# Performance work log

Hardware: AMD Instinct MI355X
Metric: run time of the kernel (lower is better)

## Reference

```python
import jax, jax.numpy as jnp
import numpy as np

K = 1024        # num_embeddings
D = 256         # embedding_dim
B, T = 64, 512  # batch, time -> N = 32768 flattened vectors
S = 5           # num_samples
DECAY = 0.999
EPS = 1e-5
COMMIT = 0.25


def setup_inputs() -> dict:
    key = jax.random.key(0)
    k1, k2 = jax.random.split(key)
    x = jax.random.normal(k1, (B, T, D), dtype=jnp.float32)
    # nn.init.uniform_(weight, -1/512, 1/512)
    embedding = jax.random.uniform(k2, (K, D), dtype=jnp.float32, minval=-1.0 / 512, maxval=1.0 / 512)
    ema_count = jnp.zeros((K,), dtype=jnp.float32)
    ema_weight = embedding  # buffer initialized as a clone of the weight
    return {"x": x, "embedding": embedding, "ema_count": ema_count, "ema_weight": ema_weight}


def reference(x, embedding, ema_count, ema_weight):
    N = x.shape[0] * x.shape[1]
    xf = x.reshape(-1, D)                      # [N, D]
    xf_sg = jax.lax.stop_gradient(xf)
    w = jax.lax.stop_gradient(embedding)       # [K, D]

    distances = (jnp.sum(w * w, axis=1)[None, :]
                 + jnp.sum(xf_sg * xf_sg, axis=1, keepdims=True)
                 - 2.0 * (xf_sg @ w.T))

    # categorical sampling with logits = -distances, S samples per row -> [S, N]
    skey = jax.random.key(42)
    samples = jax.random.categorical(skey, -distances, axis=-1, shape=(S, N))

    # mean of S one-hots without materializing [S, N, K] one-hot tensor
    encodings = jnp.zeros((N, K), dtype=jnp.float32).at[jnp.arange(N)[None, :], samples].add(1.0 / S)

    # EMA codebook update (training path; all under no_grad in torch)
    new_count = DECAY * ema_count + (1.0 - DECAY) * jnp.sum(encodings, axis=0)
    n = jnp.sum(new_count)
    new_count = (new_count + EPS) / (n + K * EPS) * n
    dw = encodings.T @ xf_sg                   # [K, D]
    new_weight = DECAY * ema_weight + (1.0 - DECAY) * dw
    new_embedding = new_weight / new_count[:, None]

    # gather with the UPDATED codebook, mean over samples -> [N, D]
    quantized = jnp.mean(new_embedding[samples], axis=0).reshape(x.shape)
    quantized = jax.lax.stop_gradient(quantized)

    e_latent_loss = jnp.mean((x - quantized) ** 2)
    loss = COMMIT * e_latent_loss

    quantized_st = x + jax.lax.stop_gradient(quantized - x)  # straight-through

    avg_probs = jnp.mean(encodings, axis=0)
    perplexity = jnp.exp(-jnp.sum(avg_probs * jnp.log(avg_probs + 1e-10)))

    return quantized_st, loss, perplexity, new_embedding, new_count, new_weight
```

## Files before the change

kernel.cpp:

```cpp
#include <hip/hip_runtime.h>
#include <stdint.h>
#include <math.h>

#define NV 32768
#define DIM 256
#define KCB 1024
#define NSAMP 5

typedef double f64x4 __attribute__((ext_vector_type(4)));

__device__ __forceinline__ uint32_t rotl32(uint32_t v, int r) {
  return (v << r) | (v >> (32 - r));
}

__device__ __forceinline__ void threefry2x32(uint32_t c0, uint32_t c1,
                                             uint32_t& o0, uint32_t& o1) {
  const uint32_t k0 = 0u, k1 = 42u;
  const uint32_t k2 = k0 ^ k1 ^ 0x1BD11BDAu;
  uint32_t x0 = c0 + k0, x1 = c1 + k1;
  x0 += x1; x1 = rotl32(x1, 13); x1 ^= x0;
  x0 += x1; x1 = rotl32(x1, 15); x1 ^= x0;
  x0 += x1; x1 = rotl32(x1, 26); x1 ^= x0;
  x0 += x1; x1 = rotl32(x1,  6); x1 ^= x0;
  x0 += k1; x1 += k2 + 1u;
  x0 += x1; x1 = rotl32(x1, 17); x1 ^= x0;
  x0 += x1; x1 = rotl32(x1, 29); x1 ^= x0;
  x0 += x1; x1 = rotl32(x1, 16); x1 ^= x0;
  x0 += x1; x1 = rotl32(x1, 24); x1 ^= x0;
  x0 += k2; x1 += k0 + 2u;
  x0 += x1; x1 = rotl32(x1, 13); x1 ^= x0;
  x0 += x1; x1 = rotl32(x1, 15); x1 ^= x0;
  x0 += x1; x1 = rotl32(x1, 26); x1 ^= x0;
  x0 += x1; x1 = rotl32(x1,  6); x1 ^= x0;
  x0 += k0; x1 += k1 + 3u;
  x0 += x1; x1 = rotl32(x1, 17); x1 ^= x0;
  x0 += x1; x1 = rotl32(x1, 29); x1 ^= x0;
  x0 += x1; x1 = rotl32(x1, 16); x1 ^= x0;
  x0 += x1; x1 = rotl32(x1, 24); x1 ^= x0;
  x0 += k1; x1 += k2 + 4u;
  x0 += x1; x1 = rotl32(x1, 13); x1 ^= x0;
  x0 += x1; x1 = rotl32(x1, 15); x1 ^= x0;
  x0 += x1; x1 = rotl32(x1, 26); x1 ^= x0;
  x0 += x1; x1 = rotl32(x1,  6); x1 ^= x0;
  x0 += k2; x1 += k0 + 5u;
  o0 = x0; o1 = x1;
}

__device__ __forceinline__ float neg_log_f32(float xf) {
  uint32_t i = __float_as_uint(xf);
  int e = ((int)(i - 0x3f3504f3u)) >> 23;
  double m = (double)__uint_as_float(i - (uint32_t)(e << 23));
  double z = (m - 1.0) / (m + 1.0);
  double p = z * z;
  double poly = 0x1.1111111111111p-4;
  poly = fma(poly, p, 0x1.3b13b13b13b14p-4);
  poly = fma(poly, p, 0x1.745d1745d1746p-4);
  poly = fma(poly, p, 0x1.c71c71c71c71cp-4);
  poly = fma(poly, p, 0x1.2492492492492p-3);
  poly = fma(poly, p, 0x1.999999999999ap-3);
  poly = fma(poly, p, 0x1.5555555555555p-2);
  poly = fma(poly, p, 1.0);
  double r = fma(-2.0 * z, poly, (double)(-e) * 0x1.62e42fefa39efp-1);
  return (float)r;
}

__device__ __forceinline__ float u_from_bits(uint32_t bits) {
  uint32_t m = bits >> 9;
  return (m == 0u) ? 1.17549435e-38f
                   : (__uint_as_float(m | 0x3f800000u) - 1.0f);
}

__device__ __forceinline__ float gumbel_exact(uint32_t bits) {
  float u = u_from_bits(bits);
  float t = neg_log_f32(u);
  return neg_log_f32(t);
}

__device__ __forceinline__ float gumbel_approx(uint32_t bits) {
  float u = u_from_bits(bits);
  float t = __log2f(u) * (-0.6931471805599453f);
  return __log2f(t) * (-0.6931471805599453f);
}

#define E2G 4e-5f


__global__ __launch_bounds__(256) void k_prep32(const float* __restrict__ emb,
                                                float* __restrict__ wT) {
  __shared__ float tile[64][65];
  int bk = blockIdx.x;
  int bd = blockIdx.y;
  int t = threadIdx.x;
  int tr = t >> 6, tc = t & 63;
#pragma unroll
  for (int i = 0; i < 16; ++i) {
    int kk = tr + i * 4;
    tile[kk][tc] = emb[(size_t)(bk * 64 + kk) * 256 + bd * 64 + tc];
  }
  __syncthreads();
#pragma unroll
  for (int i = 0; i < 16; ++i) {
    int dd = tr + i * 4;
    wT[(size_t)(bd * 64 + dd) * 1024 + bk * 64 + tc] = tile[tc][dd];
  }
}

__global__ __launch_bounds__(256) void k_prep64(const float* __restrict__ emb,
                                                double* __restrict__ wT64) {
  __shared__ float tile[64][65];
  int bk = blockIdx.x;
  int bd = blockIdx.y;
  int t = threadIdx.x;
  int tr = t >> 6, tc = t & 63;
#pragma unroll
  for (int i = 0; i < 16; ++i) {
    int kk = tr + i * 4;
    tile[kk][tc] = emb[(size_t)(bk * 64 + kk) * 256 + bd * 64 + tc];
  }
  __syncthreads();
#pragma unroll
  for (int i = 0; i < 16; ++i) {
    int dd = tr + i * 4;
    wT64[(size_t)(bd * 64 + dd) * 1024 + bk * 64 + tc] = (double)tile[tc][dd];
  }
}

__global__ __launch_bounds__(256) void k_rowsumsq(const float* __restrict__ a,
                                                  float* __restrict__ outp,
                                                  int rows) {
  int r = blockIdx.x * blockDim.x + threadIdx.x;
  if (r >= rows) return;
  const float* p = a + (size_t)r * DIM;
  float acc = 0.0f;
  for (int i = 0; i < DIM; ++i) {
    float pi = p[i];
    acc = __fadd_rn(acc, __fmul_rn(pi, pi));
  }
  outp[r] = acc;
}


__global__ __launch_bounds__(256) void k_logits(const float* __restrict__ x,
                                                const float* __restrict__ wT,
                                                const float* __restrict__ wsum,
                                                const float* __restrict__ xsum,
                                                float* __restrict__ logits,
                                                int chunkbase) {
  __shared__ float xl[32 * 260];
  __shared__ float xs[32];
  int nb = blockIdx.x;
  int t = threadIdx.x;
  int lane = t & 63, wv = t >> 6;
  int m = lane & 15, g = lane >> 4;
  int rg = wv >> 1, chf = wv & 1;

#pragma unroll
  for (int i = 0; i < 32; ++i)
    xl[i * 260 + t] = x[((size_t)(chunkbase + nb * 32) + i) * 256 + t];
  if (t < 32) xs[t] = xsum[chunkbase + nb * 32 + t];
  __syncthreads();

  const float* ap = xl + (rg * 16 + m) * 260 + g;
  for (int ch = 0; ch < 4; ++ch) {
    for (int ct = 0; ct < 8; ++ct) {
      int klocal = chf * 128 + ct * 16 + m;
      int kglob = ch * 256 + klocal;
      f64x4 C = {0.0, 0.0, 0.0, 0.0};
      const float* bp = wT + (size_t)g * 1024 + kglob;
#pragma unroll 8
      for (int step = 0; step < 64; ++step) {
        double a = (double)ap[step * 4];
        double b = (double)bp[(size_t)step * 4096];
        C = __builtin_amdgcn_mfma_f64_16x16x4f64(a, b, C, 0, 0, 0);
      }
      float ws_k = wsum[kglob];
#pragma unroll
      for (int j = 0; j < 4; ++j) {
        int rloc = rg * 16 + g * 4 + j;
        float l32 = __fsub_rn(__fmul_rn(2.0f, (float)C[j]),
                              __fadd_rn(ws_k, xs[rloc]));
        logits[(size_t)(nb * 32 + rloc) * 1024 + kglob] = l32;
      }
    }
  }
}

__global__ __launch_bounds__(256) void k_sampler(const float* __restrict__ logits,
                                                 int* __restrict__ samples,
                                                 int* __restrict__ cnt,
                                                 int chunkbase) {
  int t = threadIdx.x;
  int p = t & 7;
  int rloc = blockIdx.x * 32 + (t >> 3);
  int s = blockIdx.y;
  int row = chunkbase + rloc;
  uint32_t srow = ((uint32_t)s * (uint32_t)NV + (uint32_t)row) * 1024u;

  const float4* lp = (const float4*)(logits + (size_t)rloc * 1024) + p;

  float wvt = -INFINITY, wlv = 0.f, rlv = 0.f;
  int wk = 0, rk = 0, rflag = 0;
  uint32_t wbits = 0u, rbits = 0u;

  for (int j = 0; j < 32; ++j) {
    float4 f = lp[(size_t)j * 8];
    float lvs[4] = {f.x, f.y, f.z, f.w};
    int kb = 4 * p + 32 * j;
#pragma unroll
    for (int e = 0; e < 4; ++e) {
      int k = kb + e;
      uint32_t o0, o1;
      threefry2x32(0u, srow + (uint32_t)k, o0, o1);
      uint32_t bits = o0 ^ o1;
      float vt = __fadd_rn(gumbel_approx(bits), lvs[e]);
      if (vt > wvt) {
        if (wvt > vt - E2G) {
          rk = wk; rbits = wbits; rlv = wlv; rflag = 1;
        }
        wvt = vt; wk = k; wbits = bits; wlv = lvs[e];
      } else if (vt > wvt - E2G) {
        rk = k; rbits = bits; rlv = lvs[e]; rflag = 1;
      }
    }
  }

  float ev = __fadd_rn(gumbel_exact(wbits), wlv);
  int ek = wk;
  if (rflag) {
    float er = __fadd_rn(gumbel_exact(rbits), rlv);
    if (er > ev || (er == ev && rk < ek)) { ev = er; ek = rk; }
  }
#pragma unroll
  for (int off = 1; off < 8; off <<= 1) {
    float v2 = __shfl_xor(ev, off, 64);
    int   k2 = __shfl_xor(ek, off, 64);
    if (v2 > ev || (v2 == ev && k2 < ek)) { ev = v2; ek = k2; }
  }
  if (p == 0) {
    samples[s * NV + row] = ek;
    atomicAdd(&cnt[ek], 1);
  }
}

__global__ __launch_bounds__(256) void k_fused(const float* __restrict__ x,
                                               const double* __restrict__ wT64,
                                               const float* __restrict__ wsum,
                                               const float* __restrict__ xsum,
                                               int* __restrict__ samples,
                                               int* __restrict__ cnt) {
  __shared__ float xl[16 * 260];
  __shared__ float ll[256 * 17];
  __shared__ float xs[16];
  __shared__ float vred[4 * 16 * 5];
  __shared__ int   kred[4 * 16 * 5];

  int nb = blockIdx.x;
  int t = threadIdx.x;
  int lane = t & 63, wv = t >> 6;
  int m = lane & 15, g = lane >> 4;
  int r = t & 15, kg = t >> 4;

#pragma unroll
  for (int i = 0; i < 16; ++i)
    xl[i * 260 + t] = x[((size_t)nb * 16 + i) * 256 + t];
  if (t < 16) xs[t] = xsum[nb * 16 + t];
  __syncthreads();

  float    wvt[NSAMP], wlv[NSAMP], rlv[NSAMP];
  int      wk[NSAMP], rk[NSAMP];
  uint32_t wbits[NSAMP], rbits[NSAMP];
  uint32_t rvmask = 0;
#pragma unroll
  for (int s = 0; s < NSAMP; ++s) {
    wvt[s] = -INFINITY; wlv[s] = 0.f; wk[s] = 0; wbits[s] = 0u;
    rlv[s] = 0.f; rk[s] = 0; rbits[s] = 0u;
  }
  uint32_t rowbase = ((uint32_t)nb * 16u + (uint32_t)r) * 1024u;

  for (int ch = 0; ch < 4; ++ch) {
    for (int ct = 0; ct < 4; ++ct) {
      int klocal = wv * 64 + ct * 16 + m;
      int kglob = ch * 256 + klocal;
      f64x4 C = {0.0, 0.0, 0.0, 0.0};
      const double* bp = wT64 + (size_t)g * 1024 + kglob;
      const float* ap = xl + m * 260 + g;
#pragma unroll 8
      for (int step = 0; step < 64; ++step) {
        double a = (double)ap[step * 4];
        double b = bp[(size_t)step * 4096];
        C = __builtin_amdgcn_mfma_f64_16x16x4f64(a, b, C, 0, 0, 0);
      }
      float ws_k = wsum[kglob];
#pragma unroll
      for (int j = 0; j < 4; ++j) {
        int row = g * 4 + j;
        float l32 = __fsub_rn(__fmul_rn(2.0f, (float)C[j]),
                              __fadd_rn(ws_k, xs[row]));
        ll[klocal * 17 + row] = l32;
      }
    }
    __syncthreads();
#pragma unroll 1
    for (int i = 0; i < 16; ++i) {
      int kl = kg + (i << 4);
      float lv = ll[kl * 17 + r];
      int gki = (ch << 8) + kl;
      uint32_t cbase = rowbase + (uint32_t)gki;
#pragma unroll
      for (int s = 0; s < NSAMP; ++s) {
        uint32_t o0, o1;
        threefry2x32(0u, cbase + (uint32_t)s * 33554432u, o0, o1);
        uint32_t bits = o0 ^ o1;
        float vt = __fadd_rn(gumbel_approx(bits), lv);
        if (vt > wvt[s]) {
          if (wvt[s] > vt - E2G) {
            rk[s] = wk[s]; rbits[s] = wbits[s]; rlv[s] = wlv[s];
            rvmask |= (1u << s);
          }
          wvt[s] = vt; wk[s] = gki; wbits[s] = bits; wlv[s] = lv;
        } else if (vt > wvt[s] - E2G) {
          rk[s] = gki; rbits[s] = bits; rlv[s] = lv;
          rvmask |= (1u << s);
        }
      }
    }
    __syncthreads();
  }

#pragma unroll
  for (int s = 0; s < NSAMP; ++s) {
    float ev = __fadd_rn(gumbel_exact(wbits[s]), wlv[s]);
    int ek = wk[s];
    if (rvmask & (1u << s)) {
      float er = __fadd_rn(gumbel_exact(rbits[s]), rlv[s]);
      if (er > ev || (er == ev && rk[s] < ek)) { ev = er; ek = rk[s]; }
    }
#pragma unroll
    for (int off = 16; off <= 32; off <<= 1) {
      float v2 = __shfl_xor(ev, off, 64);
      int   k2 = __shfl_xor(ek, off, 64);
      if (v2 > ev || (v2 == ev && k2 < ek)) { ev = v2; ek = k2; }
    }
    if (g == 0) {
      vred[(wv * 16 + r) * 5 + s] = ev;
      kred[(wv * 16 + r) * 5 + s] = ek;
    }
  }
  __syncthreads();
  if (t < 80) {
    int rr = t / 5, s = t % 5;
    float best = vred[rr * 5 + s];
    int bk2 = kred[rr * 5 + s];
#pragma unroll
    for (int w = 1; w < 4; ++w) {
      float v2 = vred[(w * 16 + rr) * 5 + s];
      int   k2 = kred[(w * 16 + rr) * 5 + s];
      if (v2 > best || (v2 == best && k2 < bk2)) { best = v2; bk2 = k2; }
    }
    int n = nb * 16 + rr;
    samples[s * NV + n] = bk2;
    atomicAdd(&cnt[bk2], 1);
  }
}


__global__ __launch_bounds__(1024) void k_meta(const float* __restrict__ ema_count,
                                               const int* __restrict__ cnt,
                                               int* __restrict__ offs,
                                               int* __restrict__ cursor,
                                               double* __restrict__ ncn64,
                                               float* __restrict__ out_count,
                                               float* __restrict__ out_perp) {
  __shared__ int sc[1024];
  __shared__ double red[1024];
  int k = threadIdx.x;
  int v = cnt[k];
  sc[k] = v;
  __syncthreads();
  for (int off = 1; off < 1024; off <<= 1) {
    int a = (k >= off) ? sc[k - off] : 0;
    __syncthreads();
    sc[k] += a;
    __syncthreads();
  }
  int excl = sc[k] - v;
  offs[k] = excl;
  cursor[k] = excl;

  double ec = (double)v * 0.2;
  double nc0 = 0.999 * (double)ema_count[k] + 0.001 * ec;
  red[k] = nc0;
  __syncthreads();
  for (int off = 512; off > 0; off >>= 1) {
    if (k < off) red[k] += red[k + off];
    __syncthreads();
  }
  double ntot = red[0];
  __syncthreads();
  double ncn = (nc0 + 1e-5) / (ntot + (double)KCB * 1e-5) * ntot;
  ncn64[k] = ncn;
  out_count[k] = (float)ncn;

  double avg = ec / (double)NV;
  red[k] = avg * log(avg + 1e-10);
  __syncthreads();
  for (int off = 512; off > 0; off >>= 1) {
    if (k < off) red[k] += red[k + off];
    __syncthreads();
  }
  if (k == 0) out_perp[0] = (float)exp(-red[0]);
}

__global__ __launch_bounds__(256) void k_fill(const int* __restrict__ samples,
                                              int* __restrict__ cursor,
                                              uint32_t* __restrict__ list) {
  int idx = blockIdx.x * 256 + threadIdx.x;
  int k = samples[idx];
  int n = idx & (NV - 1);
  int pos = atomicAdd(&cursor[k], 1);
  list[pos] = (uint32_t)n;
}

__global__ __launch_bounds__(256) void k_weight2(const float* __restrict__ x,
                                                 const float* __restrict__ ema_w,
                                                 const uint32_t* __restrict__ list,
                                                 const int* __restrict__ offs,
                                                 const int* __restrict__ cnt,
                                                 const double* __restrict__ ncn64,
                                                 float* __restrict__ out_w,
                                                 float* __restrict__ out_emb,
                                                 float* __restrict__ emb32) {
  int k = blockIdx.x, d = threadIdx.x;
  const uint32_t* lp = list + offs[k];
  int mcnt = cnt[k];
  double acc0 = 0.0, acc1 = 0.0;
  int i = 0;
  for (; i + 2 <= mcnt; i += 2) {
    uint32_t n0 = lp[i], n1 = lp[i + 1];
    acc0 += (double)x[(size_t)n0 * 256 + d];
    acc1 += (double)x[(size_t)n1 * 256 + d];
  }
  if (i < mcnt) acc0 += (double)x[(size_t)lp[i] * 256 + d];
  double dw = 0.2 * (acc0 + acc1);
  double nw = 0.999 * (double)ema_w[(size_t)k * 256 + d] + 0.001 * dw;
  float nw32 = (float)nw;
  float e = __fdiv_rn(nw32, (float)ncn64[k]);
  size_t i2 = (size_t)k * 256 + d;
  out_w[i2] = nw32;
  out_emb[i2] = e;
  emb32[i2] = e;
}

__global__ __launch_bounds__(256) void k_quant(const float* __restrict__ x,
                                               const int* __restrict__ samples,
                                               const float* __restrict__ emb32,
                                               float* __restrict__ out_q,
                                               double* __restrict__ lossacc) {
  __shared__ int s5[16][5];
  __shared__ double wred[4];
  int bid = blockIdx.x;
  int t = threadIdx.x;
  if (t < 80) {
    int rr = t / 5, s = t % 5;
    s5[rr][s] = samples[s * NV + bid * 16 + rr];
  }
  __syncthreads();
  double lacc = 0.0;
#pragma unroll 1
  for (int rr = 0; rr < 16; ++rr) {
    size_t n = (size_t)bid * 16 + rr;
    float xv = x[n * DIM + t];
    float acc = emb32[(size_t)s5[rr][0] * DIM + t];
#pragma unroll
    for (int s = 1; s < NSAMP; ++s)
      acc = __fadd_rn(acc, emb32[(size_t)s5[rr][s] * DIM + t]);
    float q = __fdiv_rn(acc, 5.0f);
    out_q[n * DIM + t] = __fadd_rn(xv, __fsub_rn(q, xv));
    float df = __fsub_rn(xv, q);
    lacc += (double)df * (double)df;
  }
  for (int off = 32; off > 0; off >>= 1) lacc += __shfl_down(lacc, off, 64);
  int wid = t >> 6, lane = t & 63;
  if (lane == 0) wred[wid] = lacc;
  __syncthreads();
  if (t == 0) {
    double b = wred[0] + wred[1] + wred[2] + wred[3];
    __hip_atomic_fetch_add(lossacc, b, __ATOMIC_RELAXED, __HIP_MEMORY_SCOPE_AGENT);
  }
}

__global__ void k_loss(const double* __restrict__ lossacc,
                       float* __restrict__ out_loss) {
  out_loss[0] = (float)(0.25 * (lossacc[0] / (double)(NV * DIM)));
}

extern "C" void kernel_launch(void* const* d_in, const int* in_sizes, int n_in,
                              void* d_out, int out_size, void* d_ws, size_t ws_size,
                              hipStream_t stream) {
  const float* x     = (const float*)d_in[0];
  const float* emb   = (const float*)d_in[1];
  const float* ema_c = (const float*)d_in[2];
  const float* ema_w = (const float*)d_in[3];

  float* out      = (float*)d_out;
  float* out_q    = out;
  float* out_loss = out + 8388608;
  float* out_perp = out + 8388609;
  float* out_emb  = out + 8388610;
  float* out_cnt  = out + 8650754;
  float* out_w    = out + 8651778;

  char* ws = (char*)d_ws;

  float*    wT      = (float*)(ws + 0);
  float*    wsum    = (float*)(ws + 1048576);
  float*    xsum    = (float*)(ws + 1052672);
  int*      samples = (int*)(ws + 1183744);
  int*      cnt     = (int*)(ws + 1839104);
  double*   lossacc = (double*)(ws + 1843200);
  double*   ncn64   = (double*)(ws + 1843456);
  int*      offs    = (int*)(ws + 1851648);
  int*      cursor  = (int*)(ws + 1855744);
  uint32_t* list    = (uint32_t*)(ws + 1859840);
  float*    emb32   = (float*)(ws + 2515200);
  float*    logits  = (float*)(ws + 3563776);

  size_t avail = (ws_size > 3563776) ? (ws_size - 3563776) : 0;
  size_t maxr = (avail / 4096) & ~(size_t)31;
  int chunk_rows = (maxr > (size_t)NV) ? NV : (int)maxr;
  bool split = (chunk_rows >= 8192);

  if (split) {
    hipMemsetAsync(ws + 1839104, 0, 4096 + 8, stream);
    k_prep32<<<dim3(16, 4), 256, 0, stream>>>(emb, wT);
    k_rowsumsq<<<KCB / 256, 256, 0, stream>>>(emb, wsum, KCB);
    k_rowsumsq<<<NV / 256, 256, 0, stream>>>(x, xsum, NV);
    for (int base = 0; base < NV; base += chunk_rows) {
      int rows = (NV - base < chunk_rows) ? (NV - base) : chunk_rows;
      k_logits<<<rows / 32, 256, 0, stream>>>(x, wT, wsum, xsum, logits, base);
      k_sampler<<<dim3(rows / 32, 5), 256, 0, stream>>>(logits, samples, cnt, base);
    }
    k_meta<<<1, 1024, 0, stream>>>(ema_c, cnt, offs, cursor, ncn64,
                                   out_cnt, out_perp);
    k_fill<<<NV * NSAMP / 256, 256, 0, stream>>>(samples, cursor, list);
    k_weight2<<<KCB, 256, 0, stream>>>(x, ema_w, list, offs, cnt, ncn64,
                                       out_w, out_emb, emb32);
    k_quant<<<NV / 16, 256, 0, stream>>>(x, samples, emb32, out_q, lossacc);
    k_loss<<<1, 1, 0, stream>>>(lossacc, out_loss);
  } else {
    double*   wT64_f    = (double*)(ws + 0);
    float*    wsum_f    = (float*)(ws + 2097152);
    float*    xsum_f    = (float*)(ws + 2101248);
    int*      samples_f = (int*)(ws + 2232320);
    int*      cnt_f     = (int*)(ws + 2887680);
    double*   lossacc_f = (double*)(ws + 2891776);
    double*   ncn64_f   = (double*)(ws + 2891784);
    int*      offs_f    = (int*)(ws + 2899976);
    int*      cursor_f  = (int*)(ws + 2904072);
    uint32_t* list_f    = (uint32_t*)(ws + 2908168);
    float*    emb32_f   = (float*)(ws + 3563528);

    hipMemsetAsync(ws + 2887680, 0, 4096 + 8, stream);
    k_prep64<<<dim3(16, 4), 256, 0, stream>>>(emb, wT64_f);
    k_rowsumsq<<<KCB / 256, 256, 0, stream>>>(emb, wsum_f, KCB);
    k_rowsumsq<<<NV / 256, 256, 0, stream>>>(x, xsum_f, NV);
    k_fused<<<NV / 16, 256, 0, stream>>>(x, wT64_f, wsum_f, xsum_f,
                                         samples_f, cnt_f);
    k_meta<<<1, 1024, 0, stream>>>(ema_c, cnt_f, offs_f, cursor_f, ncn64_f,
                                   out_cnt, out_perp);
    k_fill<<<NV * NSAMP / 256, 256, 0, stream>>>(samples_f, cursor_f, list_f);
    k_weight2<<<KCB, 256, 0, stream>>>(x, ema_w, list_f, offs_f, cnt_f, ncn64_f,
                                       out_w, out_emb, emb32_f);
    k_quant<<<NV / 16, 256, 0, stream>>>(x, samples_f, emb32_f, out_q, lossacc_f);
    k_loss<<<1, 1, 0, stream>>>(lossacc_f, out_loss);
  }
}
```

Baseline: 924.9 us.

## Process all samples per sampler thread and fuse row norms into logits kernel

```diff
diff --git a/kernel.cpp b/kernel.cpp
--- a/kernel.cpp
+++ b/kernel.cpp
@@ -143,7 +143,6 @@
 __global__ __launch_bounds__(256) void k_logits(const float* __restrict__ x,
                                                 const float* __restrict__ wT,
                                                 const float* __restrict__ wsum,
-                                                const float* __restrict__ xsum,
                                                 float* __restrict__ logits,
                                                 int chunkbase) {
   __shared__ float xl[32 * 260];
@@ -157,7 +156,17 @@
 #pragma unroll
   for (int i = 0; i < 32; ++i)
     xl[i * 260 + t] = x[((size_t)(chunkbase + nb * 32) + i) * 256 + t];
-  if (t < 32) xs[t] = xsum[chunkbase + nb * 32 + t];
+  __syncthreads();
+
+  if (t < 32) {
+    const float* p = xl + t * 260;
+    float acc = 0.0f;
+    for (int i = 0; i < DIM; ++i) {
+      float pi = p[i];
+      acc = __fadd_rn(acc, __fmul_rn(pi, pi));
+    }
+    xs[t] = acc;
+  }
   __syncthreads();
 
   const float* ap = xl + (rg * 16 + m) * 260 + g;
@@ -192,16 +201,22 @@
   int t = threadIdx.x;
   int p = t & 7;
   int rloc = blockIdx.x * 32 + (t >> 3);
-  int s = blockIdx.y;
   int row = chunkbase + rloc;
-  uint32_t srow = ((uint32_t)s * (uint32_t)NV + (uint32_t)row) * 1024u;
+  uint32_t rowk = (uint32_t)row * 1024u;
 
   const float4* lp = (const float4*)(logits + (size_t)rloc * 1024) + p;
 
-  float wvt = -INFINITY, wlv = 0.f, rlv = 0.f;
-  int wk = 0, rk = 0, rflag = 0;
-  uint32_t wbits = 0u, rbits = 0u;
-
+  float    wvt[NSAMP], wlv[NSAMP], rlv[NSAMP];
+  int      wk[NSAMP], rk[NSAMP];
+  uint32_t wbits[NSAMP], rbits[NSAMP];
+  uint32_t rmask = 0;
+#pragma unroll
+  for (int s = 0; s < NSAMP; ++s) {
+    wvt[s] = -INFINITY; wlv[s] = 0.f; wk[s] = 0; wbits[s] = 0u;
+    rlv[s] = 0.f; rk[s] = 0; rbits[s] = 0u;
+  }
+
+#pragma unroll 1
   for (int j = 0; j < 32; ++j) {
     float4 f = lp[(size_t)j * 8];
     float lvs[4] = {f.x, f.y, f.z, f.w};
@@ -209,36 +224,47 @@
 #pragma unroll
     for (int e = 0; e < 4; ++e) {
       int k = kb + e;
-      uint32_t o0, o1;
-      threefry2x32(0u, srow + (uint32_t)k, o0, o1);
-      uint32_t bits = o0 ^ o1;
-      float vt = __fadd_rn(gumbel_approx(bits), lvs[e]);
-      if (vt > wvt) {
-        if (wvt > vt - E2G) {
-          rk = wk; rbits = wbits; rlv = wlv; rflag = 1;
+      float lv = lvs[e];
+      uint32_t cbase = rowk + (uint32_t)k;
+#pragma unroll
+      for (int s = 0; s < NSAMP; ++s) {
+        uint32_t o0, o1;
+        threefry2x32(0u, cbase + (uint32_t)s * 33554432u, o0, o1);
+        uint32_t bits = o0 ^ o1;
+        float vt = __fadd_rn(gumbel_approx(bits), lv);
+        float wpre = wvt[s];
+        if (fminf(vt, wpre) > fmaxf(vt, wpre) - E2G) {
+          if (vt > wpre) { rk[s] = wk[s]; rbits[s] = wbits[s]; rlv[s] = wlv[s]; }
+          else           { rk[s] = k;     rbits[s] = bits;     rlv[s] = lv; }
+          rmask |= (1u << s);
         }
-        wvt = vt; wk = k; wbits = bits; wlv = lvs[e];
-      } else if (vt > wvt - E2G) {
-        rk = k; rbits = bits; rlv = lvs[e]; rflag = 1;
+        bool gt = vt > wpre;
+        wvt[s]   = gt ? vt   : wpre;
+        wk[s]    = gt ? k    : wk[s];
+        wbits[s] = gt ? bits : wbits[s];
+        wlv[s]   = gt ? lv   : wlv[s];
       }
     }
   }
 
-  float ev = __fadd_rn(gumbel_exact(wbits), wlv);
-  int ek = wk;
-  if (rflag) {
-    float er = __fadd_rn(gumbel_exact(rbits), rlv);
-    if (er > ev || (er == ev && rk < ek)) { ev = er; ek = rk; }
-  }
-#pragma unroll
-  for (int off = 1; off < 8; off <<= 1) {
-    float v2 = __shfl_xor(ev, off, 64);
-    int   k2 = __shfl_xor(ek, off, 64);
-    if (v2 > ev || (v2 == ev && k2 < ek)) { ev = v2; ek = k2; }
-  }
-  if (p == 0) {
-    samples[s * NV + row] = ek;
-    atomicAdd(&cnt[ek], 1);
+#pragma unroll
+  for (int s = 0; s < NSAMP; ++s) {
+    float ev = __fadd_rn(gumbel_exact(wbits[s]), wlv[s]);
+    int ek = wk[s];
+    if (rmask & (1u << s)) {
+      float er = __fadd_rn(gumbel_exact(rbits[s]), rlv[s]);
+      if (er > ev || (er == ev && rk[s] < ek)) { ev = er; ek = rk[s]; }
+    }
+#pragma unroll
+    for (int off = 1; off < 8; off <<= 1) {
+      float v2 = __shfl_xor(ev, off, 64);
+      int   k2 = __shfl_xor(ek, off, 64);
+      if (v2 > ev || (v2 == ev && k2 < ek)) { ev = v2; ek = k2; }
+    }
+    if (p == 0) {
+      samples[s * NV + row] = ek;
+      atomicAdd(&cnt[ek], 1);
+    }
   }
 }
 
@@ -534,11 +560,10 @@
     hipMemsetAsync(ws + 1839104, 0, 4096 + 8, stream);
     k_prep32<<<dim3(16, 4), 256, 0, stream>>>(emb, wT);
     k_rowsumsq<<<KCB / 256, 256, 0, stream>>>(emb, wsum, KCB);
-    k_rowsumsq<<<NV / 256, 256, 0, stream>>>(x, xsum, NV);
     for (int base = 0; base < NV; base += chunk_rows) {
       int rows = (NV - base < chunk_rows) ? (NV - base) : chunk_rows;
-      k_logits<<<rows / 32, 256, 0, stream>>>(x, wT, wsum, xsum, logits, base);
-      k_sampler<<<dim3(rows / 32, 5), 256, 0, stream>>>(logits, samples, cnt, base);
+      k_logits<<<rows / 32, 256, 0, stream>>>(x, wT, wsum, logits, base);
+      k_sampler<<<rows / 32, 256, 0, stream>>>(logits, samples, cnt, base);
     }
     k_meta<<<1, 1024, 0, stream>>>(ema_c, cnt, offs, cursor, ncn64,
                                    out_cnt, out_perp);
```

New measurement: 862.3 us. -6.8%, faster.
